# Kernel optimization log

Measured on AMD Instinct MI355X. Metric: run time of the kernel, lower is better.

The kernel has to match this reference:

```python
import jax, jax.numpy as jnp
import numpy as np

N_IN, N_OUT, F, H, E, V = 80, 25, 4096, 512, 512, 4096
B = 128
BOS = V - 3  # vocab = sorted words + ['<PAD>', '<BOS>', '<EOS>', '<UNK>']
LEAK = 0.01  # torch leaky_relu default slope


def gru_cell(x, h, wih, whh, bih, bhh):
    # PyTorch GRU gate order: [r, z, n]
    gi = x @ wih.T + bih
    gh = h @ whh.T + bhh
    ir, iz, inn = jnp.split(gi, 3, axis=-1)
    hr, hz, hn = jnp.split(gh, 3, axis=-1)
    r = jax.nn.sigmoid(ir + hr)
    z = jax.nn.sigmoid(iz + hz)
    n = jnp.tanh(inn + r * hn)
    return (1.0 - z) * n + z * h


def run_gru(xs, h0, wih, whh, bih, bhh):
    # xs: [T, B, D] -> outputs [T, B, H], final hidden [B, H]
    def step(h, x):
        h2 = gru_cell(x, h, wih, whh, bih, bhh)
        return h2, h2
    hT, ys = jax.lax.scan(step, h0, xs)
    return ys, hT


def setup_inputs() -> dict:
    key = jax.random.key(0)
    ks = jax.random.split(key, 10)

    def w(k, shape, fan_in):
        return jax.random.normal(k, shape, dtype=jnp.float32) / np.float32(np.sqrt(fan_in))

    return {
        "feats": jax.random.normal(ks[0], (N_IN, B, F), dtype=jnp.float32),
        "fc_w": w(ks[1], (E, F), F),
        "fc_b": jnp.zeros((E,), jnp.float32),
        "enc_wih": w(ks[2], (3 * H, E), E),
        "enc_whh": w(ks[3], (3 * H, H), H),
        "enc_bih": jnp.zeros((3 * H,), jnp.float32),
        "enc_bhh": jnp.zeros((3 * H,), jnp.float32),
        "dec_wih": w(ks[4], (3 * H, 2 * H + E), 2 * H + E),
        "dec_whh": w(ks[5], (3 * H, H), H),
        "dec_bih": jnp.zeros((3 * H,), jnp.float32),
        "dec_bhh": jnp.zeros((3 * H,), jnp.float32),
        "out_w": w(ks[6], (V, H), H),
        "out_b": jnp.zeros((V,), jnp.float32),
        "embed": jax.random.normal(ks[7], (V, E), dtype=jnp.float32) * 0.05,
        "tgt": jax.random.randint(ks[8], (B, N_OUT), 0, V, dtype=jnp.int32),
        "tfr": 0,
    }


def reference(feats, fc_w, fc_b, enc_wih, enc_whh, enc_bih, enc_bhh,
              dec_wih, dec_whh, dec_bih, dec_bhh, out_w, out_b, embed,
              tgt, tfr):
    T_in, Bv, _ = feats.shape
    # fc + leaky_relu (dropout = identity in eval)
    xp = jax.nn.leaky_relu(feats @ fc_w.T + fc_b, LEAK)            # [T_in, B, E]
    e_seq = jnp.concatenate([xp, jnp.zeros((N_OUT, Bv, E), xp.dtype)], axis=0)
    h0 = jnp.zeros((Bv, H), xp.dtype)
    enc_out, _ = run_gru(e_seq, h0, enc_wih, enc_whh, enc_bih, enc_bhh)  # [T_in+N_OUT, B, H]
    encA = jnp.transpose(enc_out[:T_in], (1, 0, 2))                # [B, T_in, H]
    # decoder pass 1 over encoding stage: input = [zeros(H+E) ; enc_out]
    dec1_in = jnp.concatenate(
        [jnp.zeros((T_in, Bv, H + E), xp.dtype), enc_out[:T_in]], axis=-1)
    _, alpha = run_gru(dec1_in, h0, dec_wih, dec_whh, dec_bih, dec_bhh)  # [B, H]

    d0 = jnp.broadcast_to(embed[BOS], (Bv, E))                     # <BOS> embedding
    enc_tail = enc_out[T_in:T_in + N_OUT]                          # [N_OUT, B, H]
    tgt_T = tgt.T                                                  # [N_OUT, B]

    def step(carry, inp):
        h, d = carry
        et_j, t_j = inp
        # dot-product attention over the T_in encoder states (Att_ linear is unused)
        s = jnp.tanh(jnp.einsum('bih,bh->bi', encA, h))            # [B, T_in]
        w = jax.nn.softmax(s, axis=1)
        c = jnp.einsum('bi,bih->bh', w, encA)                      # [B, H]
        x = jnp.concatenate([d, et_j, c], axis=-1)                 # [B, E+2H]
        h2 = gru_cell(x, h, dec_wih, dec_whh, dec_bih, dec_bhh)
        logp = jax.nn.log_softmax(h2 @ out_w.T + out_b, axis=-1)   # [B, V]
        lj = -jnp.mean(jnp.take_along_axis(logp, t_j[:, None], axis=1))
        d_next = embed[jnp.argmax(logp, axis=-1)]                  # greedy feedback (tfr=-1)
        return (h2, d_next), lj

    _, losses = jax.lax.scan(step, (alpha, d0), (enc_tail, tgt_T))
    return jnp.sum(losses) / N_OUT
```

## Files before the change

### kernel.cpp

```cpp
#include <hip/hip_runtime.h>
#include <hip/hip_bf16.h>

#define N_IN  80
#define N_OUT 25
#define BOS   4093

typedef __attribute__((ext_vector_type(8))) short bf16x8;
typedef __attribute__((ext_vector_type(4))) float f32x4;

__device__ inline unsigned short f2bf(float f) {
    unsigned int u = __builtin_bit_cast(unsigned int, f);
    unsigned int r = (u + 0x7fffu + ((u >> 16) & 1u)) >> 16;
    return (unsigned short)r;
}
__device__ inline float bf2f(unsigned short s) {
    return __builtin_bit_cast(float, (unsigned int)s << 16);
}
__device__ inline float sigf(float x) { return 1.f / (1.f + expf(-x)); }

__device__ __forceinline__ unsigned long long ld_u64_coh(const void* p) {
    return __hip_atomic_load((const unsigned long long*)p, __ATOMIC_RELAXED, __HIP_MEMORY_SCOPE_AGENT);
}
__device__ __forceinline__ void st_u64_coh(void* p, unsigned long long v) {
    __hip_atomic_store((unsigned long long*)p, v, __ATOMIC_RELAXED, __HIP_MEMORY_SCOPE_AGENT);
}
__device__ __forceinline__ float ld_f32_coh(const float* p) {
    unsigned int u = __hip_atomic_load((const unsigned int*)p, __ATOMIC_RELAXED, __HIP_MEMORY_SCOPE_AGENT);
    return __builtin_bit_cast(float, u);
}
__device__ __forceinline__ void st_f32_coh(float* p, float v) {
    __hip_atomic_store((unsigned int*)p, __builtin_bit_cast(unsigned int, v), __ATOMIC_RELAXED, __HIP_MEMORY_SCOPE_AGENT);
}
__device__ __forceinline__ void st_u16_coh(unsigned short* p, unsigned short v) {
    __hip_atomic_store(p, v, __ATOMIC_RELAXED, __HIP_MEMORY_SCOPE_AGENT);
}
__device__ __forceinline__ int ld_i32_coh(const int* p) {
    return __hip_atomic_load(p, __ATOMIC_RELAXED, __HIP_MEMORY_SCOPE_AGENT);
}
__device__ __forceinline__ void st_i32_coh(int* p, int v) {
    __hip_atomic_store(p, v, __ATOMIC_RELAXED, __HIP_MEMORY_SCOPE_AGENT);
}
__device__ __forceinline__ bf16x8 ld_bf8_coh(const unsigned short* p) {
    union { unsigned long long u[2]; bf16x8 v; } r;
    r.u[0] = ld_u64_coh(p);
    r.u[1] = ld_u64_coh(p + 4);
    return r.v;
}
__device__ inline unsigned long long pack_ff(float a, float b) {
    return ((unsigned long long)__builtin_bit_cast(unsigned int, b) << 32) |
           __builtin_bit_cast(unsigned int, a);
}
__device__ inline unsigned long long pack_if(int a, float b) {
    return ((unsigned long long)__builtin_bit_cast(unsigned int, b) << 32) |
           (unsigned int)a;
}

__device__ __forceinline__ void spin_ge(const int* p, int tgt)
{
    while (ld_i32_coh(p) < tgt) __builtin_amdgcn_s_sleep(1);
}

template<int AFP32, int OUT_BF, int ACT>
__global__ __launch_bounds__(256)
void gemm_mfma(const void* __restrict__ Ap, int lda,
               const unsigned short* __restrict__ W, int ldw,
               const float* __restrict__ bias,
               void* __restrict__ Cp, int ldc, int K)
{
    __shared__ short Abuf[128 * 32];
    __shared__ short Wbuf[128 * 32];
    const int tid  = threadIdx.x;
    const int lane = tid & 63;
    const int wave = tid >> 6;
    const int wr = wave >> 1, wc = wave & 1;
    const int l15 = lane & 15, kg = lane >> 4;
    const int m0 = blockIdx.y * 128, n0 = blockIdx.x * 128;

    const float* Af = (const float*)Ap;
    const unsigned short* Ab = (const unsigned short*)Ap;

    f32x4 acc[4][4];
#pragma unroll
    for (int i = 0; i < 4; ++i)
#pragma unroll
        for (int j = 0; j < 4; ++j) acc[i][j] = f32x4{0.f, 0.f, 0.f, 0.f};

    const bf16x8* Av = (const bf16x8*)Abuf;
    const bf16x8* Wv = (const bf16x8*)Wbuf;

    for (int k0 = 0; k0 < K; k0 += 32) {
#pragma unroll
        for (int cc = 0; cc < 2; ++cc) {
            int c = tid + cc * 256;
            int row = c >> 2, k8 = (c & 3) * 8;
            if (AFP32) {
                const float* src = &Af[(size_t)(m0 + row) * lda + k0 + k8];
                float4 v0 = *reinterpret_cast<const float4*>(src);
                float4 v1 = *reinterpret_cast<const float4*>(src + 4);
                bf16x8 s;
                s[0] = (short)f2bf(v0.x); s[1] = (short)f2bf(v0.y);
                s[2] = (short)f2bf(v0.z); s[3] = (short)f2bf(v0.w);
                s[4] = (short)f2bf(v1.x); s[5] = (short)f2bf(v1.y);
                s[6] = (short)f2bf(v1.z); s[7] = (short)f2bf(v1.w);
                *reinterpret_cast<bf16x8*>(&Abuf[row * 32 + k8]) = s;
            } else {
                *reinterpret_cast<bf16x8*>(&Abuf[row * 32 + k8]) =
                    *reinterpret_cast<const bf16x8*>(&Ab[(size_t)(m0 + row) * lda + k0 + k8]);
            }
            *reinterpret_cast<bf16x8*>(&Wbuf[row * 32 + k8]) =
                *reinterpret_cast<const bf16x8*>(&W[(size_t)(n0 + row) * ldw + k0 + k8]);
        }
        __syncthreads();
        bf16x8 a[4], b[4];
#pragma unroll
        for (int i = 0; i < 4; ++i) a[i] = Av[(wr * 64 + i * 16 + l15) * 4 + kg];
#pragma unroll
        for (int j = 0; j < 4; ++j) b[j] = Wv[(wc * 64 + j * 16 + l15) * 4 + kg];
#pragma unroll
        for (int i = 0; i < 4; ++i)
#pragma unroll
            for (int j = 0; j < 4; ++j)
                acc[i][j] = __builtin_amdgcn_mfma_f32_16x16x32_bf16(a[i], b[j], acc[i][j], 0, 0, 0);
        __syncthreads();
    }

    float* Cf = (float*)Cp;
    unsigned short* Cb = (unsigned short*)Cp;
#pragma unroll
    for (int i = 0; i < 4; ++i) {
#pragma unroll
        for (int j = 0; j < 4; ++j) {
            int n = n0 + wc * 64 + j * 16 + l15;
            float bv = bias[n];
#pragma unroll
            for (int r = 0; r < 4; ++r) {
                int m = m0 + wr * 64 + i * 16 + kg * 4 + r;
                float v = acc[i][j][r] + bv;
                if (ACT == 1) v = v > 0.f ? v : 0.01f * v;
                if (OUT_BF) Cb[(size_t)m * ldc + n] = f2bf(v);
                else        Cf[(size_t)m * ldc + n] = v;
            }
        }
    }
}

__global__ __launch_bounds__(256, 1)
void recur_persist(const unsigned short* __restrict__ enc_gi_bf,
                   const float* __restrict__ enc_bih, const float* __restrict__ enc_bhh,
                   const unsigned short* __restrict__ encwhh_bf,
                   const unsigned short* __restrict__ decwih_bf,
                   const unsigned short* __restrict__ decwhh_bf,
                   const float* __restrict__ dec_bih, const float* __restrict__ dec_bhh,
                   const unsigned short* __restrict__ h0b,
                   float* __restrict__ enc_out, unsigned short* __restrict__ encout_bf,
                   float* __restrict__ hDf, unsigned short* __restrict__ hDb,
                   int* efl, int* dfl)
{
    const int g = blockIdx.x;
    const int tid = threadIdx.x, w = tid >> 6, lane = tid & 63;
    const int l15 = lane & 15, kg = lane >> 4;

    if (g < 32) {
        const int cg = g >> 1, rh = g & 1;
        const int mb = rh * 64 + w * 16;
        int wrow[6];
#pragma unroll
        for (int ct = 0; ct < 6; ++ct) wrow[ct] = (ct >> 1) * 512 + cg * 32 + (ct & 1) * 16 + l15;

        for (int i = 0; i < 105; ++i) {
            if (i > 0) {
                if (tid < 32) spin_ge(&efl[tid * 32], i);
                __syncthreads();
                asm volatile("" ::: "memory");
            }
            const unsigned short* A = (i == 0) ? h0b : encout_bf + (size_t)(i - 1) * 65536;
            bf16x8 areg[16];
#pragma unroll
            for (int ks = 0; ks < 16; ++ks)
                areg[ks] = ld_bf8_coh(&A[(size_t)(mb + l15) * 512 + ks * 32 + kg * 8]);
            f32x4 acc[6];
#pragma unroll
            for (int ct = 0; ct < 6; ++ct) acc[ct] = f32x4{0.f, 0.f, 0.f, 0.f};
#pragma unroll
            for (int ks = 0; ks < 16; ++ks) {
#pragma unroll
                for (int ct = 0; ct < 6; ++ct) {
                    bf16x8 bv = *(const bf16x8*)&encwhh_bf[(size_t)wrow[ct] * 512 + ks * 32 + kg * 8];
                    acc[ct] = __builtin_amdgcn_mfma_f32_16x16x32_bf16(areg[ks], bv, acc[ct], 0, 0, 0);
                }
            }
#pragma unroll
            for (int jh = 0; jh < 2; ++jh) {
                int jc = cg * 32 + jh * 16 + l15;
                float bhr = enc_bhh[jc], bhz = enc_bhh[512 + jc], bhn = enc_bhh[1024 + jc];
#pragma unroll
                for (int rr = 0; rr < 4; ++rr) {
                    int br = mb + kg * 4 + rr;
                    float gr_, gz_, gn_;
                    if (i < 80) {
                        const unsigned short* gp = enc_gi_bf + ((size_t)i * 128 + br) * 1536 + jc;
                        gr_ = bf2f(gp[0]); gz_ = bf2f(gp[512]); gn_ = bf2f(gp[1024]);
                    } else {
                        gr_ = enc_bih[jc]; gz_ = enc_bih[512 + jc]; gn_ = enc_bih[1024 + jc];
                    }
                    float hp = (i == 0) ? 0.f : enc_out[(size_t)(i - 1) * 65536 + br * 512 + jc];
                    float r = sigf(gr_ + bhr + acc[jh][rr]);
                    float z = sigf(gz_ + bhz + acc[2 + jh][rr]);
                    float n = tanhf(gn_ + r * (acc[4 + jh][rr] + bhn));
                    float v = (1.f - z) * n + z * hp;
                    enc_out[(size_t)i * 65536 + br * 512 + jc] = v;
                    st_u16_coh(&encout_bf[(size_t)i * 65536 + br * 512 + jc], f2bf(v));
                }
            }
            __syncthreads();
            if (tid == 0) st_i32_coh(&efl[g * 32], i + 1);
        }
    } else {
        const int gl = g - 32, cg = gl >> 2, rq = gl & 3;
        const int rt = w >> 1, cs = w & 1;
        const int mb = rq * 32 + rt * 16;
        int wrow[3];
#pragma unroll
        for (int t = 0; t < 3; ++t) wrow[t] = t * 512 + cg * 32 + cs * 16 + l15;
        const int jc = cg * 32 + cs * 16 + l15;

        for (int i = 1; i <= 80; ++i) {
            if (tid < 32) spin_ge(&efl[tid * 32], i);
            else if (tid < 96 && i >= 2) spin_ge(&dfl[(tid - 32) * 32], i - 1);
            __syncthreads();
            asm volatile("" ::: "memory");

            f32x4 agi[3], agh[3];
#pragma unroll
            for (int t = 0; t < 3; ++t) { agi[t] = f32x4{0.f,0.f,0.f,0.f}; agh[t] = f32x4{0.f,0.f,0.f,0.f}; }
            bf16x8 areg[16];
            const unsigned short* A1 = encout_bf + (size_t)(i - 1) * 65536;
#pragma unroll
            for (int ks = 0; ks < 16; ++ks)
                areg[ks] = ld_bf8_coh(&A1[(size_t)(mb + l15) * 512 + ks * 32 + kg * 8]);
#pragma unroll
            for (int ks = 0; ks < 16; ++ks) {
#pragma unroll
                for (int t = 0; t < 3; ++t) {
                    bf16x8 bv = *(const bf16x8*)&decwih_bf[(size_t)wrow[t] * 1536 + 1024 + ks * 32 + kg * 8];
                    agi[t] = __builtin_amdgcn_mfma_f32_16x16x32_bf16(areg[ks], bv, agi[t], 0, 0, 0);
                }
            }
            const unsigned short* A2 = (i == 1) ? h0b : hDb + (size_t)((i - 1) & 1) * 65536;
#pragma unroll
            for (int ks = 0; ks < 16; ++ks)
                areg[ks] = ld_bf8_coh(&A2[(size_t)(mb + l15) * 512 + ks * 32 + kg * 8]);
#pragma unroll
            for (int ks = 0; ks < 16; ++ks) {
#pragma unroll
                for (int t = 0; t < 3; ++t) {
                    bf16x8 bv = *(const bf16x8*)&decwhh_bf[(size_t)wrow[t] * 512 + ks * 32 + kg * 8];
                    agh[t] = __builtin_amdgcn_mfma_f32_16x16x32_bf16(areg[ks], bv, agh[t], 0, 0, 0);
                }
            }
            float bir = dec_bih[jc], bhr = dec_bhh[jc];
            float biz = dec_bih[512 + jc], bhz = dec_bhh[512 + jc];
            float bin_ = dec_bih[1024 + jc], bhn = dec_bhh[1024 + jc];
            const float* hpf = hDf + (size_t)((i - 1) & 1) * 65536;
            float* hof = hDf + (size_t)(i & 1) * 65536;
            unsigned short* hob = hDb + (size_t)(i & 1) * 65536;
#pragma unroll
            for (int rr = 0; rr < 4; ++rr) {
                int br = mb + kg * 4 + rr;
                float hp = (i == 1) ? 0.f : hpf[br * 512 + jc];
                float r = sigf(agi[0][rr] + bir + agh[0][rr] + bhr);
                float z = sigf(agi[1][rr] + biz + agh[1][rr] + bhz);
                float n = tanhf(agi[2][rr] + bin_ + r * (agh[2][rr] + bhn));
                float v = (1.f - z) * n + z * hp;
                hof[br * 512 + jc] = v;
                st_u16_coh(&hob[br * 512 + jc], f2bf(v));
            }
            __syncthreads();
            if (tid == 0) st_i32_coh(&dfl[gl * 32], i);
        }
    }
}

__device__ void attention(int b, const float* __restrict__ hvec,
                          unsigned short* __restrict__ c_bf,
                          float* hsh, float* ssh, const unsigned short* esh)
{
    const int tid = threadIdx.x;
    hsh[tid]       = ld_f32_coh(&hvec[(size_t)b * 512 + tid]);
    hsh[256 + tid] = ld_f32_coh(&hvec[(size_t)b * 512 + 256 + tid]);
    __syncthreads();
    const int wv = tid >> 6, lane = tid & 63;
    float hreg[8];
#pragma unroll
    for (int q = 0; q < 8; ++q) hreg[q] = hsh[lane * 8 + q];
#pragma unroll 4
    for (int i = wv; i < 80; i += 4) {
        bf16x8 v = *(const bf16x8*)&esh[i * 512 + lane * 8];
        float p = 0.f;
#pragma unroll
        for (int q = 0; q < 8; ++q) p += bf2f((unsigned short)v[q]) * hreg[q];
#pragma unroll
        for (int off = 32; off > 0; off >>= 1) p += __shfl_xor(p, off, 64);
        if (lane == 0) ssh[i] = tanhf(p);
    }
    __syncthreads();
    if (tid == 0) {
        float mx = -1e30f;
        for (int i = 0; i < 80; ++i) mx = fmaxf(mx, ssh[i]);
        float s = 0.f;
        for (int i = 0; i < 80; ++i) { float e = expf(ssh[i] - mx); ssh[i] = e; s += e; }
        ssh[80] = 1.0f / s;
    }
    __syncthreads();
    float acc0 = 0.f, acc1 = 0.f;
    const unsigned short* ebase = esh + tid * 2;
#pragma unroll 10
    for (int i = 0; i < 80; ++i) {
        unsigned int u = *reinterpret_cast<const unsigned int*>(&ebase[i * 512]);
        float w = ssh[i];
        acc0 += w * __builtin_bit_cast(float, u << 16);
        acc1 += w * __builtin_bit_cast(float, u & 0xffff0000u);
    }
    float inv = ssh[80];
    st_u16_coh(&c_bf[(size_t)b * 512 + tid * 2],     f2bf(acc0 * inv));
    st_u16_coh(&c_bf[(size_t)b * 512 + tid * 2 + 1], f2bf(acc1 * inv));
    __syncthreads();
}

__global__ __launch_bounds__(256, 1)
void decode_persist(const unsigned short* __restrict__ encout_bf,
                    const unsigned short* __restrict__ decwih_bf, const unsigned short* __restrict__ decwhh_bf,
                    const float* __restrict__ dec_bhh,
                    const unsigned short* __restrict__ outw_bf, const float* __restrict__ out_b,
                    const unsigned short* __restrict__ emb2gi, const float* __restrict__ gie,
                    const int* __restrict__ tgt,
                    const float* __restrict__ hDf, const unsigned short* __restrict__ hDb,
                    float* __restrict__ hCf, unsigned short* __restrict__ hCb,
                    unsigned short* __restrict__ c_bf, int* __restrict__ argidx,
                    unsigned long long* __restrict__ pA, unsigned long long* __restrict__ pB,
                    float* __restrict__ out,
                    int* c1, int* cp, int* c2, int* c3)
{
    __shared__ unsigned short esh[80 * 512];
    __shared__ float hsh[512];
    __shared__ float ssh[88];
    __shared__ float sM[128];
    __shared__ int   sI[128];
    __shared__ float sL[128];

    const int g = blockIdx.x;
    const int tid = threadIdx.x, w = tid >> 6, lane = tid & 63;
    const int l15 = lane & 15, kg = lane >> 4;
    float loss_acc = 0.f;

    for (int i = w; i < 80; i += 4)
        *(bf16x8*)&esh[i * 512 + lane * 8] =
            *(const bf16x8*)&encout_bf[(size_t)i * 65536 + g * 512 + lane * 8];
    __syncthreads();

    attention(g, hDf, c_bf, hsh, ssh, esh);
    if (tid == 0) st_i32_coh(&argidx[g], BOS);
    __syncthreads();
    if (tid == 0) st_i32_coh(&c2[g * 32], 1);

    for (int j = 0; j < 25; ++j) {
        const unsigned short* h_in_b = (j == 0) ? hDb : hCb + (size_t)((j - 1) & 1) * 65536;
        const float* h_in_f = (j == 0) ? hDf : hCf + (size_t)((j - 1) & 1) * 65536;
        float* h_out_f = hCf + (size_t)(j & 1) * 65536;
        unsigned short* h_out_b = hCb + (size_t)(j & 1) * 65536;

        if (g < 64) {
            if (tid < 128) spin_ge(&c3[tid * 32], j);
            else           spin_ge(&c2[(tid - 128) * 32], j + 1);
            __syncthreads();
            asm volatile("" ::: "memory");

            const int cg = g >> 2, rq = g & 3;
            const int rt = w >> 1, cs = w & 1;
            const int mb = rq * 32 + rt * 16;
            const int jc = cg * 32 + cs * 16 + l15;
            int wrow[3];
#pragma unroll
            for (int t = 0; t < 3; ++t) wrow[t] = t * 512 + cg * 32 + cs * 16 + l15;

            f32x4 agi[3], agh[3];
#pragma unroll
            for (int t = 0; t < 3; ++t) { agi[t] = f32x4{0.f,0.f,0.f,0.f}; agh[t] = f32x4{0.f,0.f,0.f,0.f}; }
            bf16x8 areg[16];

#pragma unroll
            for (int ks = 0; ks < 16; ++ks)
                areg[ks] = ld_bf8_coh(&c_bf[(size_t)(mb + l15) * 512 + ks * 32 + kg * 8]);
#pragma unroll
            for (int ks = 0; ks < 16; ++ks)
#pragma unroll
                for (int t = 0; t < 3; ++t) {
                    bf16x8 bv = *(const bf16x8*)&decwih_bf[(size_t)wrow[t] * 1536 + 1024 + ks * 32 + kg * 8];
                    agi[t] = __builtin_amdgcn_mfma_f32_16x16x32_bf16(areg[ks], bv, agi[t], 0, 0, 0);
                }
#pragma unroll
            for (int ks = 0; ks < 16; ++ks)
                areg[ks] = ld_bf8_coh(&h_in_b[(size_t)(mb + l15) * 512 + ks * 32 + kg * 8]);
#pragma unroll
            for (int ks = 0; ks < 16; ++ks)
#pragma unroll
                for (int t = 0; t < 3; ++t) {
                    bf16x8 bv = *(const bf16x8*)&decwhh_bf[(size_t)wrow[t] * 512 + ks * 32 + kg * 8];
                    agh[t] = __builtin_amdgcn_mfma_f32_16x16x32_bf16(areg[ks], bv, agh[t], 0, 0, 0);
                }

            float bhr = dec_bhh[jc], bhz = dec_bhh[512 + jc], bhn = dec_bhh[1024 + jc];
            int vidx[4]; float hpv[4];
#pragma unroll
            for (int rr = 0; rr < 4; ++rr) {
                int br = mb + kg * 4 + rr;
                vidx[rr] = ld_i32_coh(&argidx[br]);
                hpv[rr]  = ld_f32_coh(&h_in_f[(size_t)br * 512 + jc]);
            }
#pragma unroll
            for (int rr = 0; rr < 4; ++rr) {
                int br = mb + kg * 4 + rr;
                const float* gp = &gie[((size_t)j * 128 + br) * 1536 + jc];
                const unsigned short* ep = &emb2gi[(size_t)vidx[rr] * 1536 + jc];
                float g0 = gp[0]    + bf2f(ep[0]);
                float g1 = gp[512]  + bf2f(ep[512]);
                float g2 = gp[1024] + bf2f(ep[1024]);
                float r = sigf(g0 + agi[0][rr] + agh[0][rr] + bhr);
                float z = sigf(g1 + agi[1][rr] + agh[1][rr] + bhz);
                float n = tanhf(g2 + agi[2][rr] + r * (agh[2][rr] + bhn));
                float v = (1.f - z) * n + z * hpv[rr];
                st_f32_coh(&h_out_f[(size_t)br * 512 + jc], v);
                st_u16_coh(&h_out_b[(size_t)br * 512 + jc], f2bf(v));
            }
            __syncthreads();
            if (tid == 0) st_i32_coh(&c1[g * 32], j + 1);
        }

        {
            if (tid < 64) spin_ge(&c1[tid * 32], j + 1);
            __syncthreads();
            asm volatile("" ::: "memory");

            const int n0 = g * 32;
            f32x4 acc[2][2];
#pragma unroll
            for (int mt = 0; mt < 2; ++mt)
#pragma unroll
                for (int nt = 0; nt < 2; ++nt) acc[mt][nt] = f32x4{0.f,0.f,0.f,0.f};
            bf16x8 ar0[16], ar1[16];
#pragma unroll
            for (int ks = 0; ks < 16; ++ks)
                ar0[ks] = ld_bf8_coh(&h_out_b[(size_t)(w * 32 + l15) * 512 + ks * 32 + kg * 8]);
#pragma unroll
            for (int ks = 0; ks < 16; ++ks)
                ar1[ks] = ld_bf8_coh(&h_out_b[(size_t)(w * 32 + 16 + l15) * 512 + ks * 32 + kg * 8]);
#pragma unroll
            for (int ks = 0; ks < 16; ++ks) {
                bf16x8 b0 = *(const bf16x8*)&outw_bf[(size_t)(n0 + l15) * 512 + ks * 32 + kg * 8];
                bf16x8 b1 = *(const bf16x8*)&outw_bf[(size_t)(n0 + 16 + l15) * 512 + ks * 32 + kg * 8];
                acc[0][0] = __builtin_amdgcn_mfma_f32_16x16x32_bf16(ar0[ks], b0, acc[0][0], 0, 0, 0);
                acc[0][1] = __builtin_amdgcn_mfma_f32_16x16x32_bf16(ar0[ks], b1, acc[0][1], 0, 0, 0);
                acc[1][0] = __builtin_amdgcn_mfma_f32_16x16x32_bf16(ar1[ks], b0, acc[1][0], 0, 0, 0);
                acc[1][1] = __builtin_amdgcn_mfma_f32_16x16x32_bf16(ar1[ks], b1, acc[1][1], 0, 0, 0);
            }
            float ob0 = out_b[n0 + l15], ob1 = out_b[n0 + 16 + l15];
#pragma unroll
            for (int mt = 0; mt < 2; ++mt) {
#pragma unroll
                for (int rr = 0; rr < 4; ++rr) {
                    int m = w * 32 + mt * 16 + kg * 4 + rr;
                    float v0 = acc[mt][0][rr] + ob0;
                    float v1 = acc[mt][1][rr] + ob1;
                    int tj = tgt[m * 25 + j];
                    float pm; int pi;
                    if (v0 >= v1) { pm = v0; pi = n0 + l15; }
                    else          { pm = v1; pi = n0 + 16 + l15; }
                    float pl = -1e30f;
                    if (n0 + l15 == tj)      pl = v0;
                    if (n0 + 16 + l15 == tj) pl = v1;
#pragma unroll
                    for (int off = 1; off < 16; off <<= 1) {
                        float om = __shfl_xor(pm, off, 64);
                        int   oi = __shfl_xor(pi, off, 64);
                        float ol = __shfl_xor(pl, off, 64);
                        if (om > pm || (om == pm && oi < pi)) { pm = om; pi = oi; }
                        pl = fmaxf(pl, ol);
                    }
                    float ps = expf(v0 - pm) + expf(v1 - pm);
#pragma unroll
                    for (int off = 1; off < 16; off <<= 1) ps += __shfl_xor(ps, off, 64);
                    if (l15 == 0) {
                        st_u64_coh(&pA[(size_t)m * 128 + g], pack_ff(pm, ps));
                        st_u64_coh(&pB[(size_t)m * 128 + g], pack_if(pi, pl));
                    }
                }
            }
            __syncthreads();
            if (tid == 0) st_i32_coh(&cp[g * 32], j + 1);
            if (j < 24) attention(g, h_out_f, c_bf, hsh, ssh, esh);
            __syncthreads();
            if (tid == 0) st_i32_coh(&c2[g * 32], j + 2);
        }

        {
            if (tid < 128) spin_ge(&cp[tid * 32], j + 1);
            __syncthreads();
            asm volatile("" ::: "memory");

            const int b = g;
            float m_ = -1e30f, s_ = 0.f, l_ = -1e30f; int i_ = 0x7fffffff;
            if (tid < 128) {
                unsigned long long ua = ld_u64_coh(&pA[(size_t)b * 128 + tid]);
                unsigned long long ub = ld_u64_coh(&pB[(size_t)b * 128 + tid]);
                m_ = __builtin_bit_cast(float, (unsigned int)ua);
                s_ = __builtin_bit_cast(float, (unsigned int)(ua >> 32));
                i_ = (int)(unsigned int)ub;
                l_ = __builtin_bit_cast(float, (unsigned int)(ub >> 32));
            }
            if (tid < 128) { sM[tid] = m_; sI[tid] = i_; sL[tid] = l_; }
            __syncthreads();
            for (int s = 64; s > 0; s >>= 1) {
                if (tid < s) {
                    float om = sM[tid + s]; int oi = sI[tid + s];
                    if (om > sM[tid] || (om == sM[tid] && oi < sI[tid])) { sM[tid] = om; sI[tid] = oi; }
                    sL[tid] = fmaxf(sL[tid], sL[tid + s]);
                }
                __syncthreads();
            }
            float M = sM[0]; float LT = sL[0];
            int gidx = sI[0];
            __syncthreads();
            if (tid < 128) sM[tid] = s_ * expf(m_ - M);
            __syncthreads();
            for (int s = 64; s > 0; s >>= 1) {
                if (tid < s) sM[tid] += sM[tid + s];
                __syncthreads();
            }
            if (tid == 0) {
                float lse = M + logf(sM[0]);
                loss_acc += -(LT - lse);
                st_i32_coh(&argidx[b], gidx);
            }
            __syncthreads();
            if (tid == 0) st_i32_coh(&c3[g * 32], j + 1);
        }
    }

    if (tid == 0) atomicAdd(out, loss_acc * (1.0f / 3200.0f));
}

__global__ void cast_f2b(const float* __restrict__ in, unsigned short* __restrict__ out, int n)
{
    int i = (blockIdx.x * 256 + threadIdx.x) * 4;
    if (i < n) {
        float4 v = *reinterpret_cast<const float4*>(&in[i]);
        out[i + 0] = f2bf(v.x); out[i + 1] = f2bf(v.y);
        out[i + 2] = f2bf(v.z); out[i + 3] = f2bf(v.w);
    }
}

extern "C" void kernel_launch(void* const* d_in, const int* in_sizes, int n_in,
                              void* d_out, int out_size, void* d_ws, size_t ws_size,
                              hipStream_t stream)
{
    const float* feats   = (const float*)d_in[0];
    const float* fc_w    = (const float*)d_in[1];
    const float* fc_b    = (const float*)d_in[2];
    const float* enc_wih = (const float*)d_in[3];
    const float* enc_whh = (const float*)d_in[4];
    const float* enc_bih = (const float*)d_in[5];
    const float* enc_bhh = (const float*)d_in[6];
    const float* dec_wih = (const float*)d_in[7];
    const float* dec_whh = (const float*)d_in[8];
    const float* dec_bih = (const float*)d_in[9];
    const float* dec_bhh = (const float*)d_in[10];
    const float* out_w   = (const float*)d_in[11];
    const float* out_b   = (const float*)d_in[12];
    const float* embed   = (const float*)d_in[13];
    const int*   tgt     = (const int*)d_in[14];

    float* ws = (float*)d_ws;
    size_t off = 0;
    auto afl = [&](size_t n) { float* r = ws + off; off += n; return r; };

    unsigned short* enc_gi_bf = (unsigned short*)afl(7864320);
    float* enc_out           = afl(6881280);
    unsigned short* encout_bf = (unsigned short*)afl(3440640);
    unsigned short* xp_bf     = (unsigned short*)afl(2621440);
    unsigned short* fcw_bf    = (unsigned short*)afl(1048576);
    unsigned short* encwih_bf = (unsigned short*)afl(393216);
    unsigned short* encwhh_bf = (unsigned short*)afl(393216);
    unsigned short* decwih_bf = (unsigned short*)afl(1179648);
    unsigned short* decwhh_bf = (unsigned short*)afl(393216);
    unsigned short* outw_bf   = (unsigned short*)afl(1048576);
    unsigned short* embed_bf  = (unsigned short*)afl(1048576);
    unsigned short* emb2gi    = (unsigned short*)afl(3145728);
    float* gie               = afl(4915200);
    float* zbias             = afl(1536);
    unsigned short* h0b       = (unsigned short*)afl(32768);
    float* hDf               = afl(131072);
    unsigned short* hDb       = (unsigned short*)afl(65536);
    float* hCf               = afl(131072);
    unsigned short* hCb       = (unsigned short*)afl(65536);
    unsigned short* c_bf      = (unsigned short*)afl(32768);
    int* argidx              = (int*)afl(128);
    unsigned long long* pA   = (unsigned long long*)afl(32768);
    unsigned long long* pB   = (unsigned long long*)afl(32768);
    int* flags               = (int*)afl(32768);

    int* efl = flags;
    int* dfl = flags + 32 * 32;
    int* c1  = flags + 96 * 32;
    int* cp  = flags + 224 * 32;
    int* c2  = flags + 352 * 32;
    int* c3  = flags + 480 * 32;

    hipMemsetAsync(h0b, 0, 65536 * sizeof(unsigned short), stream);
    hipMemsetAsync(zbias, 0, 1536 * sizeof(float), stream);
    hipMemsetAsync(flags, 0, 32768 * sizeof(int), stream);
    hipMemsetAsync(d_out, 0, sizeof(float), stream);

    cast_f2b<<<2048, 256, 0, stream>>>(fc_w, fcw_bf, 2097152);
    cast_f2b<<<768, 256, 0, stream>>>(enc_wih, encwih_bf, 786432);
    cast_f2b<<<768, 256, 0, stream>>>(enc_whh, encwhh_bf, 786432);
    cast_f2b<<<2304, 256, 0, stream>>>(dec_wih, decwih_bf, 2359296);
    cast_f2b<<<768, 256, 0, stream>>>(dec_whh, decwhh_bf, 786432);
    cast_f2b<<<2048, 256, 0, stream>>>(out_w, outw_bf, 2097152);
    cast_f2b<<<2048, 256, 0, stream>>>(embed, embed_bf, 2097152);

    gemm_mfma<1, 1, 1><<<dim3(4, 80), 256, 0, stream>>>(feats, 4096, fcw_bf, 4096, fc_b, xp_bf, 512, 4096);
    gemm_mfma<0, 1, 0><<<dim3(12, 80), 256, 0, stream>>>(xp_bf, 512, encwih_bf, 512, enc_bih, enc_gi_bf, 1536, 512);
    gemm_mfma<0, 1, 0><<<dim3(12, 32), 256, 0, stream>>>(embed_bf, 512, decwih_bf, 1536, zbias, emb2gi, 1536, 512);

    recur_persist<<<96, 256, 0, stream>>>(enc_gi_bf, enc_bih, enc_bhh, encwhh_bf,
                                          decwih_bf, decwhh_bf, dec_bih, dec_bhh,
                                          h0b, enc_out, encout_bf, hDf, hDb,
                                          efl, dfl);

    gemm_mfma<0, 0, 0><<<dim3(12, 25), 256, 0, stream>>>(encout_bf + (size_t)80 * 65536, 512,
                                                         decwih_bf + 512, 1536, dec_bih, gie, 1536, 512);

    decode_persist<<<128, 256, 0, stream>>>(encout_bf, decwih_bf, decwhh_bf,
                                            dec_bhh, outw_bf, out_b,
                                            emb2gi, gie, tgt,
                                            hDf, hDb, hCf, hCb,
                                            c_bf, argidx, pA, pB, (float*)d_out,
                                            c1, cp, c2, c3);
}
```

Before: 4.016 ms.

## Keep hidden state in registers, coalesce state stores, remove argmax sync stage

Each recurrent block now keeps its previous hidden values in registers instead of re-reading fp32 copies, and drops the fp32 state buffers entirely. Outputs are staged in shared memory and written as coalesced 64-bit stores. Cross-block loads use sc1 global loads with explicit waitcnt fences in place of atomic 64-bit loads. In the decoder the GRU blocks compute the greedy argmax themselves from double-buffered partials, which removes the c3 handshake and a serial reduction stage per step. The cost is that attention and the next step now read the hidden state in bf16 instead of fp32, a small precision change, and the correctness of the sc1 coherence rests on the inline assembly.

```diff
diff --git a/kernel.cpp b/kernel.cpp
--- a/kernel.cpp
+++ b/kernel.cpp
@@ -1,7 +1,6 @@
 #include <hip/hip_runtime.h>
 #include <hip/hip_bf16.h>
 
-#define N_IN  80
 #define N_OUT 25
 #define BOS   4093
 
@@ -24,27 +23,17 @@
 __device__ __forceinline__ void st_u64_coh(void* p, unsigned long long v) {
     __hip_atomic_store((unsigned long long*)p, v, __ATOMIC_RELAXED, __HIP_MEMORY_SCOPE_AGENT);
 }
-__device__ __forceinline__ float ld_f32_coh(const float* p) {
-    unsigned int u = __hip_atomic_load((const unsigned int*)p, __ATOMIC_RELAXED, __HIP_MEMORY_SCOPE_AGENT);
-    return __builtin_bit_cast(float, u);
-}
-__device__ __forceinline__ void st_f32_coh(float* p, float v) {
-    __hip_atomic_store((unsigned int*)p, __builtin_bit_cast(unsigned int, v), __ATOMIC_RELAXED, __HIP_MEMORY_SCOPE_AGENT);
-}
-__device__ __forceinline__ void st_u16_coh(unsigned short* p, unsigned short v) {
-    __hip_atomic_store(p, v, __ATOMIC_RELAXED, __HIP_MEMORY_SCOPE_AGENT);
+__device__ __forceinline__ void st_u32_coh(void* p, unsigned int v) {
+    __hip_atomic_store((unsigned int*)p, v, __ATOMIC_RELAXED, __HIP_MEMORY_SCOPE_AGENT);
+}
+__device__ __forceinline__ unsigned short ld_u16_coh(const unsigned short* p) {
+    return __hip_atomic_load(p, __ATOMIC_RELAXED, __HIP_MEMORY_SCOPE_AGENT);
 }
 __device__ __forceinline__ int ld_i32_coh(const int* p) {
     return __hip_atomic_load(p, __ATOMIC_RELAXED, __HIP_MEMORY_SCOPE_AGENT);
 }
 __device__ __forceinline__ void st_i32_coh(int* p, int v) {
     __hip_atomic_store(p, v, __ATOMIC_RELAXED, __HIP_MEMORY_SCOPE_AGENT);
-}
-__device__ __forceinline__ bf16x8 ld_bf8_coh(const unsigned short* p) {
-    union { unsigned long long u[2]; bf16x8 v; } r;
-    r.u[0] = ld_u64_coh(p);
-    r.u[1] = ld_u64_coh(p + 4);
-    return r.v;
 }
 __device__ inline unsigned long long pack_ff(float a, float b) {
     return ((unsigned long long)__builtin_bit_cast(unsigned int, b) << 32) |
@@ -54,11 +43,18 @@
     return ((unsigned long long)__builtin_bit_cast(unsigned int, b) << 32) |
            (unsigned int)a;
 }
-
 __device__ __forceinline__ void spin_ge(const int* p, int tgt)
 {
     while (ld_i32_coh(p) < tgt) __builtin_amdgcn_s_sleep(1);
 }
+
+__device__ __forceinline__ bf16x8 ld_bf8_sc1(const unsigned short* p) {
+    bf16x8 r;
+    asm volatile("global_load_dwordx4 %0, %1, off sc1" : "=v"(r) : "v"(p));
+    return r;
+}
+#define VM_FENCE do { asm volatile("s_waitcnt vmcnt(0)" ::: "memory"); \
+                      __builtin_amdgcn_sched_barrier(0); } while (0)
 
 template<int AFP32, int OUT_BF, int ACT>
 __global__ __launch_bounds__(256)
@@ -151,11 +147,12 @@
                    const unsigned short* __restrict__ decwih_bf,
                    const unsigned short* __restrict__ decwhh_bf,
                    const float* __restrict__ dec_bih, const float* __restrict__ dec_bhh,
-                   const unsigned short* __restrict__ h0b,
-                   float* __restrict__ enc_out, unsigned short* __restrict__ encout_bf,
-                   float* __restrict__ hDf, unsigned short* __restrict__ hDb,
+                   unsigned short* __restrict__ encout_bf,
+                   unsigned short* __restrict__ hDb,
                    int* efl, int* dfl)
 {
+    __shared__ unsigned long long tileq[512];
+    unsigned short* tile16 = (unsigned short*)tileq;
     const int g = blockIdx.x;
     const int tid = threadIdx.x, w = tid >> 6, lane = tid & 63;
     const int l15 = lane & 15, kg = lane >> 4;
@@ -166,6 +163,7 @@
         int wrow[6];
 #pragma unroll
         for (int ct = 0; ct < 6; ++ct) wrow[ct] = (ct >> 1) * 512 + cg * 32 + (ct & 1) * 16 + l15;
+        float hreg[2][4] = {{0.f,0.f,0.f,0.f},{0.f,0.f,0.f,0.f}};
 
         for (int i = 0; i < 105; ++i) {
             if (i > 0) {
@@ -173,11 +171,17 @@
                 __syncthreads();
                 asm volatile("" ::: "memory");
             }
-            const unsigned short* A = (i == 0) ? h0b : encout_bf + (size_t)(i - 1) * 65536;
             bf16x8 areg[16];
-#pragma unroll
-            for (int ks = 0; ks < 16; ++ks)
-                areg[ks] = ld_bf8_coh(&A[(size_t)(mb + l15) * 512 + ks * 32 + kg * 8]);
+            if (i > 0) {
+                const unsigned short* ap = &encout_bf[(size_t)(i - 1) * 65536 + (size_t)(mb + l15) * 512 + kg * 8];
+                VM_FENCE;
+#pragma unroll
+                for (int ks = 0; ks < 16; ++ks) areg[ks] = ld_bf8_sc1(ap + ks * 32);
+                VM_FENCE;
+            } else {
+#pragma unroll
+                for (int ks = 0; ks < 16; ++ks) areg[ks] = bf16x8{0,0,0,0,0,0,0,0};
+            }
             f32x4 acc[6];
 #pragma unroll
             for (int ct = 0; ct < 6; ++ct) acc[ct] = f32x4{0.f, 0.f, 0.f, 0.f};
@@ -203,30 +207,38 @@
                     } else {
                         gr_ = enc_bih[jc]; gz_ = enc_bih[512 + jc]; gn_ = enc_bih[1024 + jc];
                     }
-                    float hp = (i == 0) ? 0.f : enc_out[(size_t)(i - 1) * 65536 + br * 512 + jc];
                     float r = sigf(gr_ + bhr + acc[jh][rr]);
                     float z = sigf(gz_ + bhz + acc[2 + jh][rr]);
                     float n = tanhf(gn_ + r * (acc[4 + jh][rr] + bhn));
-                    float v = (1.f - z) * n + z * hp;
-                    enc_out[(size_t)i * 65536 + br * 512 + jc] = v;
-                    st_u16_coh(&encout_bf[(size_t)i * 65536 + br * 512 + jc], f2bf(v));
-                }
+                    float v = (1.f - z) * n + z * hreg[jh][rr];
+                    hreg[jh][rr] = v;
+                    tile16[(w * 16 + kg * 4 + rr) * 32 + jh * 16 + l15] = f2bf(v);
+                }
+            }
+            __syncthreads();
+            {
+                size_t base = (size_t)i * 65536 + (size_t)(rh * 64) * 512 + cg * 32;
+                int row = tid >> 3, ch = tid & 7;
+                st_u64_coh(&encout_bf[base + (size_t)row * 512 + ch * 4], tileq[tid]);
+                st_u64_coh(&encout_bf[base + (size_t)(32 + row) * 512 + ch * 4], tileq[256 + tid]);
             }
             __syncthreads();
             if (tid == 0) st_i32_coh(&efl[g * 32], i + 1);
         }
     } else {
-        const int gl = g - 32, cg = gl >> 2, rq = gl & 3;
+        const int s = g - 32;
+        const int cg = s >> 2, rq = s & 3;
         const int rt = w >> 1, cs = w & 1;
         const int mb = rq * 32 + rt * 16;
         int wrow[3];
 #pragma unroll
         for (int t = 0; t < 3; ++t) wrow[t] = t * 512 + cg * 32 + cs * 16 + l15;
         const int jc = cg * 32 + cs * 16 + l15;
+        float hreg[4] = {0.f, 0.f, 0.f, 0.f};
 
         for (int i = 1; i <= 80; ++i) {
             if (tid < 32) spin_ge(&efl[tid * 32], i);
-            else if (tid < 96 && i >= 2) spin_ge(&dfl[(tid - 32) * 32], i - 1);
+            else if (tid >= 64 && tid < 128 && i >= 2) spin_ge(&dfl[(tid - 64) * 32], i - 1);
             __syncthreads();
             asm volatile("" ::: "memory");
 
@@ -234,60 +246,73 @@
 #pragma unroll
             for (int t = 0; t < 3; ++t) { agi[t] = f32x4{0.f,0.f,0.f,0.f}; agh[t] = f32x4{0.f,0.f,0.f,0.f}; }
             bf16x8 areg[16];
-            const unsigned short* A1 = encout_bf + (size_t)(i - 1) * 65536;
+            {
+                const unsigned short* ap = &encout_bf[(size_t)(i - 1) * 65536 + (size_t)(mb + l15) * 512 + kg * 8];
+                VM_FENCE;
+#pragma unroll
+                for (int ks = 0; ks < 16; ++ks) areg[ks] = ld_bf8_sc1(ap + ks * 32);
+                VM_FENCE;
+            }
 #pragma unroll
             for (int ks = 0; ks < 16; ++ks)
-                areg[ks] = ld_bf8_coh(&A1[(size_t)(mb + l15) * 512 + ks * 32 + kg * 8]);
-#pragma unroll
-            for (int ks = 0; ks < 16; ++ks) {
 #pragma unroll
                 for (int t = 0; t < 3; ++t) {
                     bf16x8 bv = *(const bf16x8*)&decwih_bf[(size_t)wrow[t] * 1536 + 1024 + ks * 32 + kg * 8];
                     agi[t] = __builtin_amdgcn_mfma_f32_16x16x32_bf16(areg[ks], bv, agi[t], 0, 0, 0);
                 }
-            }
-            const unsigned short* A2 = (i == 1) ? h0b : hDb + (size_t)((i - 1) & 1) * 65536;
+            if (i >= 2) {
+                const unsigned short* ap = &hDb[(size_t)((i - 1) & 1) * 65536 + (size_t)(mb + l15) * 512 + kg * 8];
+                VM_FENCE;
+#pragma unroll
+                for (int ks = 0; ks < 16; ++ks) areg[ks] = ld_bf8_sc1(ap + ks * 32);
+                VM_FENCE;
+            } else {
+#pragma unroll
+                for (int ks = 0; ks < 16; ++ks) areg[ks] = bf16x8{0,0,0,0,0,0,0,0};
+            }
 #pragma unroll
             for (int ks = 0; ks < 16; ++ks)
-                areg[ks] = ld_bf8_coh(&A2[(size_t)(mb + l15) * 512 + ks * 32 + kg * 8]);
-#pragma unroll
-            for (int ks = 0; ks < 16; ++ks) {
 #pragma unroll
                 for (int t = 0; t < 3; ++t) {
                     bf16x8 bv = *(const bf16x8*)&decwhh_bf[(size_t)wrow[t] * 512 + ks * 32 + kg * 8];
                     agh[t] = __builtin_amdgcn_mfma_f32_16x16x32_bf16(areg[ks], bv, agh[t], 0, 0, 0);
                 }
-            }
             float bir = dec_bih[jc], bhr = dec_bhh[jc];
             float biz = dec_bih[512 + jc], bhz = dec_bhh[512 + jc];
             float bin_ = dec_bih[1024 + jc], bhn = dec_bhh[1024 + jc];
-            const float* hpf = hDf + (size_t)((i - 1) & 1) * 65536;
-            float* hof = hDf + (size_t)(i & 1) * 65536;
-            unsigned short* hob = hDb + (size_t)(i & 1) * 65536;
 #pragma unroll
             for (int rr = 0; rr < 4; ++rr) {
-                int br = mb + kg * 4 + rr;
-                float hp = (i == 1) ? 0.f : hpf[br * 512 + jc];
                 float r = sigf(agi[0][rr] + bir + agh[0][rr] + bhr);
                 float z = sigf(agi[1][rr] + biz + agh[1][rr] + bhz);
                 float n = tanhf(agi[2][rr] + bin_ + r * (agh[2][rr] + bhn));
-                float v = (1.f - z) * n + z * hp;
-                hof[br * 512 + jc] = v;
-                st_u16_coh(&hob[br * 512 + jc], f2bf(v));
-            }
-            __syncthreads();
-            if (tid == 0) st_i32_coh(&dfl[gl * 32], i);
+                float v = (1.f - z) * n + z * hreg[rr];
+                hreg[rr] = v;
+                tile16[(rt * 16 + kg * 4 + rr) * 32 + cs * 16 + l15] = f2bf(v);
+            }
+            __syncthreads();
+            {
+                size_t base = (size_t)(i & 1) * 65536 + (size_t)(rq * 32) * 512 + cg * 32;
+                int row = tid >> 3, ch = tid & 7;
+                st_u64_coh(&hDb[base + (size_t)row * 512 + ch * 4], tileq[tid]);
+            }
+            __syncthreads();
+            if (tid == 0) st_i32_coh(&dfl[s * 32], i);
         }
     }
 }
 
-__device__ void attention(int b, const float* __restrict__ hvec,
+__device__ void attention(int b, const unsigned short* __restrict__ hrow,
                           unsigned short* __restrict__ c_bf,
                           float* hsh, float* ssh, const unsigned short* esh)
 {
     const int tid = threadIdx.x;
-    hsh[tid]       = ld_f32_coh(&hvec[(size_t)b * 512 + tid]);
-    hsh[256 + tid] = ld_f32_coh(&hvec[(size_t)b * 512 + 256 + tid]);
+    if (tid < 128) {
+        unsigned long long u = ld_u64_coh(&hrow[tid * 4]);
+        hsh[tid * 4 + 0] = bf2f((unsigned short)(u));
+        hsh[tid * 4 + 1] = bf2f((unsigned short)(u >> 16));
+        hsh[tid * 4 + 2] = bf2f((unsigned short)(u >> 32));
+        hsh[tid * 4 + 3] = bf2f((unsigned short)(u >> 48));
+    }
     __syncthreads();
     const int wv = tid >> 6, lane = tid & 63;
     float hreg[8];
@@ -322,8 +347,8 @@
         acc1 += w * __builtin_bit_cast(float, u & 0xffff0000u);
     }
     float inv = ssh[80];
-    st_u16_coh(&c_bf[(size_t)b * 512 + tid * 2],     f2bf(acc0 * inv));
-    st_u16_coh(&c_bf[(size_t)b * 512 + tid * 2 + 1], f2bf(acc1 * inv));
+    unsigned int packed = (unsigned int)f2bf(acc0 * inv) | ((unsigned int)f2bf(acc1 * inv) << 16);
+    st_u32_coh(&c_bf[(size_t)b * 512 + tid * 2], packed);
     __syncthreads();
 }
 
@@ -334,19 +359,22 @@
                     const unsigned short* __restrict__ outw_bf, const float* __restrict__ out_b,
                     const unsigned short* __restrict__ emb2gi, const float* __restrict__ gie,
                     const int* __restrict__ tgt,
-                    const float* __restrict__ hDf, const unsigned short* __restrict__ hDb,
-                    float* __restrict__ hCf, unsigned short* __restrict__ hCb,
-                    unsigned short* __restrict__ c_bf, int* __restrict__ argidx,
+                    const unsigned short* __restrict__ hDb,
+                    unsigned short* __restrict__ hCb,
+                    unsigned short* __restrict__ c_bf,
                     unsigned long long* __restrict__ pA, unsigned long long* __restrict__ pB,
                     float* __restrict__ out,
-                    int* c1, int* cp, int* c2, int* c3)
+                    int* c1, int* cp, int* c2)
 {
     __shared__ unsigned short esh[80 * 512];
     __shared__ float hsh[512];
     __shared__ float ssh[88];
-    __shared__ float sM[128];
-    __shared__ int   sI[128];
-    __shared__ float sL[128];
+    __shared__ unsigned long long tileq[256];
+    __shared__ float sMv[256];
+    __shared__ int   sIv[256];
+    __shared__ float sLv[256];
+    __shared__ int   sVid[32];
+    unsigned short* tile16 = (unsigned short*)tileq;
 
     const int g = blockIdx.x;
     const int tid = threadIdx.x, w = tid >> 6, lane = tid & 63;
@@ -358,39 +386,50 @@
             *(const bf16x8*)&encout_bf[(size_t)i * 65536 + g * 512 + lane * 8];
     __syncthreads();
 
-    attention(g, hDf, c_bf, hsh, ssh, esh);
-    if (tid == 0) st_i32_coh(&argidx[g], BOS);
+    attention(g, hDb + (size_t)g * 512, c_bf, hsh, ssh, esh);
     __syncthreads();
     if (tid == 0) st_i32_coh(&c2[g * 32], 1);
 
+    const int cg = g >> 2, rq = g & 3;
+    const int rt = w >> 1, cs = w & 1;
+    const int mb = rq * 32 + rt * 16;
+    const int jc = cg * 32 + cs * 16 + l15;
+    int wrow[3];
+#pragma unroll
+    for (int t = 0; t < 3; ++t) wrow[t] = t * 512 + cg * 32 + cs * 16 + l15;
+    float hreg[4] = {0.f, 0.f, 0.f, 0.f};
+    if (g < 64) {
+#pragma unroll
+        for (int rr = 0; rr < 4; ++rr)
+            hreg[rr] = bf2f(ld_u16_coh(&hDb[(size_t)(mb + kg * 4 + rr) * 512 + jc]));
+    }
+
     for (int j = 0; j < 25; ++j) {
         const unsigned short* h_in_b = (j == 0) ? hDb : hCb + (size_t)((j - 1) & 1) * 65536;
-        const float* h_in_f = (j == 0) ? hDf : hCf + (size_t)((j - 1) & 1) * 65536;
-        float* h_out_f = hCf + (size_t)(j & 1) * 65536;
         unsigned short* h_out_b = hCb + (size_t)(j & 1) * 65536;
+        unsigned long long* pAj = pA + (size_t)(j & 1) * 16384;
+        unsigned long long* pBj = pB + (size_t)(j & 1) * 16384;
+        const unsigned long long* pAp = pA + (size_t)((j - 1) & 1) * 16384;
+        const unsigned long long* pBp = pB + (size_t)((j - 1) & 1) * 16384;
 
         if (g < 64) {
-            if (tid < 128) spin_ge(&c3[tid * 32], j);
-            else           spin_ge(&c2[(tid - 128) * 32], j + 1);
+            if (tid < 128) spin_ge(&c2[tid * 32], j + 1);
+            else if (j >= 1) spin_ge(&cp[(tid - 128) * 32], j);
             __syncthreads();
             asm volatile("" ::: "memory");
-
-            const int cg = g >> 2, rq = g & 3;
-            const int rt = w >> 1, cs = w & 1;
-            const int mb = rq * 32 + rt * 16;
-            const int jc = cg * 32 + cs * 16 + l15;
-            int wrow[3];
-#pragma unroll
-            for (int t = 0; t < 3; ++t) wrow[t] = t * 512 + cg * 32 + cs * 16 + l15;
 
             f32x4 agi[3], agh[3];
 #pragma unroll
             for (int t = 0; t < 3; ++t) { agi[t] = f32x4{0.f,0.f,0.f,0.f}; agh[t] = f32x4{0.f,0.f,0.f,0.f}; }
             bf16x8 areg[16];
 
-#pragma unroll
-            for (int ks = 0; ks < 16; ++ks)
-                areg[ks] = ld_bf8_coh(&c_bf[(size_t)(mb + l15) * 512 + ks * 32 + kg * 8]);
+            {
+                const unsigned short* ap = &c_bf[(size_t)(mb + l15) * 512 + kg * 8];
+                VM_FENCE;
+#pragma unroll
+                for (int ks = 0; ks < 16; ++ks) areg[ks] = ld_bf8_sc1(ap + ks * 32);
+                VM_FENCE;
+            }
 #pragma unroll
             for (int ks = 0; ks < 16; ++ks)
 #pragma unroll
@@ -398,9 +437,13 @@
                     bf16x8 bv = *(const bf16x8*)&decwih_bf[(size_t)wrow[t] * 1536 + 1024 + ks * 32 + kg * 8];
                     agi[t] = __builtin_amdgcn_mfma_f32_16x16x32_bf16(areg[ks], bv, agi[t], 0, 0, 0);
                 }
-#pragma unroll
-            for (int ks = 0; ks < 16; ++ks)
-                areg[ks] = ld_bf8_coh(&h_in_b[(size_t)(mb + l15) * 512 + ks * 32 + kg * 8]);
+            {
+                const unsigned short* ap = &h_in_b[(size_t)(mb + l15) * 512 + kg * 8];
+                VM_FENCE;
+#pragma unroll
+                for (int ks = 0; ks < 16; ++ks) areg[ks] = ld_bf8_sc1(ap + ks * 32);
+                VM_FENCE;
+            }
 #pragma unroll
             for (int ks = 0; ks < 16; ++ks)
 #pragma unroll
@@ -409,28 +452,67 @@
                     agh[t] = __builtin_amdgcn_mfma_f32_16x16x32_bf16(areg[ks], bv, agh[t], 0, 0, 0);
                 }
 
+            int myvid[4];
+            if (j == 0) {
+#pragma unroll
+                for (int rr = 0; rr < 4; ++rr) myvid[rr] = BOS;
+            } else {
+                const int rowl = tid >> 3, seg = tid & 7;
+                const int browg = rq * 32 + rowl;
+                float bm = -1e30f; int bi = 0x7fffffff;
+#pragma unroll
+                for (int half = 0; half < 2; ++half) {
+                    unsigned long long ua[8], ub[8];
+#pragma unroll
+                    for (int k = 0; k < 8; ++k)
+                        ua[k] = ld_u64_coh(&pAp[(size_t)browg * 128 + seg * 16 + half * 8 + k]);
+#pragma unroll
+                    for (int k = 0; k < 8; ++k)
+                        ub[k] = ld_u64_coh(&pBp[(size_t)browg * 128 + seg * 16 + half * 8 + k]);
+#pragma unroll
+                    for (int k = 0; k < 8; ++k) {
+                        float m = __builtin_bit_cast(float, (unsigned int)ua[k]);
+                        int ii = (int)(unsigned int)ub[k];
+                        if (m > bm || (m == bm && ii < bi)) { bm = m; bi = ii; }
+                    }
+                }
+                sMv[tid] = bm; sIv[tid] = bi;
+                __syncthreads();
+                if (seg == 0) {
+                    float m = sMv[tid]; int ii = sIv[tid];
+#pragma unroll
+                    for (int k = 1; k < 8; ++k) {
+                        float om = sMv[tid + k]; int oi = sIv[tid + k];
+                        if (om > m || (om == m && oi < ii)) { m = om; ii = oi; }
+                    }
+                    sVid[rowl] = ii;
+                }
+                __syncthreads();
+#pragma unroll
+                for (int rr = 0; rr < 4; ++rr) myvid[rr] = sVid[rt * 16 + kg * 4 + rr];
+            }
+
             float bhr = dec_bhh[jc], bhz = dec_bhh[512 + jc], bhn = dec_bhh[1024 + jc];
-            int vidx[4]; float hpv[4];
-#pragma unroll
-            for (int rr = 0; rr < 4; ++rr) {
-                int br = mb + kg * 4 + rr;
-                vidx[rr] = ld_i32_coh(&argidx[br]);
-                hpv[rr]  = ld_f32_coh(&h_in_f[(size_t)br * 512 + jc]);
-            }
 #pragma unroll
             for (int rr = 0; rr < 4; ++rr) {
                 int br = mb + kg * 4 + rr;
                 const float* gp = &gie[((size_t)j * 128 + br) * 1536 + jc];
-                const unsigned short* ep = &emb2gi[(size_t)vidx[rr] * 1536 + jc];
+                const unsigned short* ep = &emb2gi[(size_t)myvid[rr] * 1536 + jc];
                 float g0 = gp[0]    + bf2f(ep[0]);
                 float g1 = gp[512]  + bf2f(ep[512]);
                 float g2 = gp[1024] + bf2f(ep[1024]);
                 float r = sigf(g0 + agi[0][rr] + agh[0][rr] + bhr);
                 float z = sigf(g1 + agi[1][rr] + agh[1][rr] + bhz);
                 float n = tanhf(g2 + agi[2][rr] + r * (agh[2][rr] + bhn));
-                float v = (1.f - z) * n + z * hpv[rr];
-                st_f32_coh(&h_out_f[(size_t)br * 512 + jc], v);
-                st_u16_coh(&h_out_b[(size_t)br * 512 + jc], f2bf(v));
+                float v = (1.f - z) * n + z * hreg[rr];
+                hreg[rr] = v;
+                tile16[(rt * 16 + kg * 4 + rr) * 32 + cs * 16 + l15] = f2bf(v);
+            }
+            __syncthreads();
+            {
+                size_t base = (size_t)(j & 1) * 65536 + (size_t)(rq * 32) * 512 + cg * 32;
+                int row = tid >> 3, ch = tid & 7;
+                st_u64_coh(&hCb[base + (size_t)row * 512 + ch * 4], tileq[tid]);
             }
             __syncthreads();
             if (tid == 0) st_i32_coh(&c1[g * 32], j + 1);
@@ -448,12 +530,16 @@
 #pragma unroll
                 for (int nt = 0; nt < 2; ++nt) acc[mt][nt] = f32x4{0.f,0.f,0.f,0.f};
             bf16x8 ar0[16], ar1[16];
-#pragma unroll
-            for (int ks = 0; ks < 16; ++ks)
-                ar0[ks] = ld_bf8_coh(&h_out_b[(size_t)(w * 32 + l15) * 512 + ks * 32 + kg * 8]);
-#pragma unroll
-            for (int ks = 0; ks < 16; ++ks)
-                ar1[ks] = ld_bf8_coh(&h_out_b[(size_t)(w * 32 + 16 + l15) * 512 + ks * 32 + kg * 8]);
+            {
+                const unsigned short* p0 = &h_out_b[(size_t)(w * 32 + l15) * 512 + kg * 8];
+                const unsigned short* p1 = &h_out_b[(size_t)(w * 32 + 16 + l15) * 512 + kg * 8];
+                VM_FENCE;
+#pragma unroll
+                for (int ks = 0; ks < 16; ++ks) ar0[ks] = ld_bf8_sc1(p0 + ks * 32);
+#pragma unroll
+                for (int ks = 0; ks < 16; ++ks) ar1[ks] = ld_bf8_sc1(p1 + ks * 32);
+                VM_FENCE;
+            }
 #pragma unroll
             for (int ks = 0; ks < 16; ++ks) {
                 bf16x8 b0 = *(const bf16x8*)&outw_bf[(size_t)(n0 + l15) * 512 + ks * 32 + kg * 8];
@@ -490,63 +576,54 @@
 #pragma unroll
                     for (int off = 1; off < 16; off <<= 1) ps += __shfl_xor(ps, off, 64);
                     if (l15 == 0) {
-                        st_u64_coh(&pA[(size_t)m * 128 + g], pack_ff(pm, ps));
-                        st_u64_coh(&pB[(size_t)m * 128 + g], pack_if(pi, pl));
+                        st_u64_coh(&pAj[(size_t)m * 128 + g], pack_ff(pm, ps));
+                        st_u64_coh(&pBj[(size_t)m * 128 + g], pack_if(pi, pl));
                     }
                 }
             }
             __syncthreads();
             if (tid == 0) st_i32_coh(&cp[g * 32], j + 1);
-            if (j < 24) attention(g, h_out_f, c_bf, hsh, ssh, esh);
+            if (j < 24) attention(g, h_out_b + (size_t)g * 512, c_bf, hsh, ssh, esh);
             __syncthreads();
             if (tid == 0) st_i32_coh(&c2[g * 32], j + 2);
         }
 
-        {
+        if (g >= 64) {
             if (tid < 128) spin_ge(&cp[tid * 32], j + 1);
             __syncthreads();
             asm volatile("" ::: "memory");
-
-            const int b = g;
-            float m_ = -1e30f, s_ = 0.f, l_ = -1e30f; int i_ = 0x7fffffff;
-            if (tid < 128) {
-                unsigned long long ua = ld_u64_coh(&pA[(size_t)b * 128 + tid]);
-                unsigned long long ub = ld_u64_coh(&pB[(size_t)b * 128 + tid]);
-                m_ = __builtin_bit_cast(float, (unsigned int)ua);
-                s_ = __builtin_bit_cast(float, (unsigned int)(ua >> 32));
-                i_ = (int)(unsigned int)ub;
-                l_ = __builtin_bit_cast(float, (unsigned int)(ub >> 32));
-            }
-            if (tid < 128) { sM[tid] = m_; sI[tid] = i_; sL[tid] = l_; }
-            __syncthreads();
-            for (int s = 64; s > 0; s >>= 1) {
-                if (tid < s) {
-                    float om = sM[tid + s]; int oi = sI[tid + s];
-                    if (om > sM[tid] || (om == sM[tid] && oi < sI[tid])) { sM[tid] = om; sI[tid] = oi; }
-                    sL[tid] = fmaxf(sL[tid], sL[tid + s]);
+            const int rowb = (g - 64) * 2 + (tid >> 7);
+            const int t2 = tid & 127;
+            unsigned long long ua = ld_u64_coh(&pAj[(size_t)rowb * 128 + t2]);
+            unsigned long long ub = ld_u64_coh(&pBj[(size_t)rowb * 128 + t2]);
+            float m_ = __builtin_bit_cast(float, (unsigned int)ua);
+            float s_ = __builtin_bit_cast(float, (unsigned int)(ua >> 32));
+            float l_ = __builtin_bit_cast(float, (unsigned int)(ub >> 32));
+            sMv[tid] = m_; sLv[tid] = l_;
+            __syncthreads();
+            for (int st = 64; st > 0; st >>= 1) {
+                if (t2 < st) {
+                    sMv[tid] = fmaxf(sMv[tid], sMv[tid + st]);
+                    sLv[tid] = fmaxf(sLv[tid], sLv[tid + st]);
                 }
                 __syncthreads();
             }
-            float M = sM[0]; float LT = sL[0];
-            int gidx = sI[0];
-            __syncthreads();
-            if (tid < 128) sM[tid] = s_ * expf(m_ - M);
-            __syncthreads();
-            for (int s = 64; s > 0; s >>= 1) {
-                if (tid < s) sM[tid] += sM[tid + s];
+            float M = sMv[tid & 128];
+            float LT = sLv[tid & 128];
+            __syncthreads();
+            sMv[tid] = s_ * expf(m_ - M);
+            __syncthreads();
+            for (int st = 64; st > 0; st >>= 1) {
+                if (t2 < st) sMv[tid] += sMv[tid + st];
                 __syncthreads();
             }
-            if (tid == 0) {
-                float lse = M + logf(sM[0]);
-                loss_acc += -(LT - lse);
-                st_i32_coh(&argidx[b], gidx);
-            }
-            __syncthreads();
-            if (tid == 0) st_i32_coh(&c3[g * 32], j + 1);
+            if (t2 == 0) loss_acc += -(LT - (M + logf(sMv[tid])));
+            __syncthreads();
         }
     }
 
-    if (tid == 0) atomicAdd(out, loss_acc * (1.0f / 3200.0f));
+    if (g >= 64 && (tid == 0 || tid == 128))
+        atomicAdd(out, loss_acc * (1.0f / 3200.0f));
 }
 
 __global__ void cast_f2b(const float* __restrict__ in, unsigned short* __restrict__ out, int n)
@@ -584,7 +661,6 @@
     auto afl = [&](size_t n) { float* r = ws + off; off += n; return r; };
 
     unsigned short* enc_gi_bf = (unsigned short*)afl(7864320);
-    float* enc_out           = afl(6881280);
     unsigned short* encout_bf = (unsigned short*)afl(3440640);
     unsigned short* xp_bf     = (unsigned short*)afl(2621440);
     unsigned short* fcw_bf    = (unsigned short*)afl(1048576);
@@ -597,27 +673,21 @@
     unsigned short* emb2gi    = (unsigned short*)afl(3145728);
     float* gie               = afl(4915200);
     float* zbias             = afl(1536);
-    unsigned short* h0b       = (unsigned short*)afl(32768);
-    float* hDf               = afl(131072);
     unsigned short* hDb       = (unsigned short*)afl(65536);
-    float* hCf               = afl(131072);
     unsigned short* hCb       = (unsigned short*)afl(65536);
     unsigned short* c_bf      = (unsigned short*)afl(32768);
-    int* argidx              = (int*)afl(128);
-    unsigned long long* pA   = (unsigned long long*)afl(32768);
-    unsigned long long* pB   = (unsigned long long*)afl(32768);
-    int* flags               = (int*)afl(32768);
+    unsigned long long* pA   = (unsigned long long*)afl(65536);
+    unsigned long long* pB   = (unsigned long long*)afl(65536);
+    int* flags               = (int*)afl(16384);
 
     int* efl = flags;
     int* dfl = flags + 32 * 32;
     int* c1  = flags + 96 * 32;
-    int* cp  = flags + 224 * 32;
-    int* c2  = flags + 352 * 32;
-    int* c3  = flags + 480 * 32;
-
-    hipMemsetAsync(h0b, 0, 65536 * sizeof(unsigned short), stream);
+    int* cp  = flags + 160 * 32;
+    int* c2  = flags + 288 * 32;
+
     hipMemsetAsync(zbias, 0, 1536 * sizeof(float), stream);
-    hipMemsetAsync(flags, 0, 32768 * sizeof(int), stream);
+    hipMemsetAsync(flags, 0, 16384 * sizeof(int), stream);
     hipMemsetAsync(d_out, 0, sizeof(float), stream);
 
     cast_f2b<<<2048, 256, 0, stream>>>(fc_w, fcw_bf, 2097152);
@@ -634,8 +704,7 @@
 
     recur_persist<<<96, 256, 0, stream>>>(enc_gi_bf, enc_bih, enc_bhh, encwhh_bf,
                                           decwih_bf, decwhh_bf, dec_bih, dec_bhh,
-                                          h0b, enc_out, encout_bf, hDf, hDb,
-                                          efl, dfl);
+                                          encout_bf, hDb, efl, dfl);
 
     gemm_mfma<0, 0, 0><<<dim3(12, 25), 256, 0, stream>>>(encout_bf + (size_t)80 * 65536, 512,
                                                          decwih_bf + 512, 1536, dec_bih, gie, 1536, 512);
@@ -643,7 +712,6 @@
     decode_persist<<<128, 256, 0, stream>>>(encout_bf, decwih_bf, decwhh_bf,
                                             dec_bhh, outw_bf, out_b,
                                             emb2gi, gie, tgt,
-                                            hDf, hDb, hCf, hCb,
-                                            c_bf, argidx, pA, pB, (float*)d_out,
-                                            c1, cp, c2, c3);
-}
+                                            hDb, hCb, c_bf, pA, pB, (float*)d_out,
+                                            c1, cp, c2);
+}
```

Measured after the change: 3.450 ms. -14.1%, faster.
